# Kernel tuning notes

Hardware: AMD Instinct MI355X
Metric: run time of the kernel (lower is better)

The kernel has to match this reference:

```python
import jax, jax.numpy as jnp
import numpy as np

DIM = 64  # per-head key dim; temp = sqrt(DIM)
B, S = 32, 2048  # flattened batch*heads, seq_len


def setup_inputs() -> dict:
    key = jax.random.key(0)
    kq, kk, kv = jax.random.split(key, 3)
    q = jax.random.normal(kq, (B, S, DIM), dtype=jnp.float32)
    k = jax.random.normal(kk, (B, S, DIM), dtype=jnp.float32)
    v = jax.random.normal(kv, (B, S, DIM), dtype=jnp.float32)
    return {"q": q, "k": k, "v": v}


def reference(q, k, v):
    temp = np.sqrt(DIM).astype(np.float32)
    # attn = bmm(q, k^T) / sqrt(dim): [B, Sq, Sk]
    attn = jnp.einsum("bqd,bkd->bqk", q, k) / temp
    # softmax over key dim (the view/softmax(dim=1)/view trick == softmax over last axis)
    attn = jax.nn.softmax(attn, axis=-1)
    # dropout p=0.0 -> identity
    out = jnp.einsum("bqk,bkd->bqd", attn, v)
    return out
```

## Files before the change

kernel.cpp:

```cpp
#include <hip/hip_runtime.h>
#include <hip/hip_bf16.h>

#define S_ 2048
#define D_ 64
#define BM 128
#define BN 128
#define KSTR 72
#define VSTR 136

typedef __attribute__((ext_vector_type(8))) short bf16x8;
typedef __attribute__((ext_vector_type(16))) float f32x16;

__device__ __forceinline__ unsigned int cvtpk(float lo, float hi) {
    unsigned int r;
    asm("v_cvt_pk_bf16_f32 %0, %1, %2" : "=v"(r) : "v"(lo), "v"(hi));
    return r;
}

__global__ __launch_bounds__(256, 2) void fattn(const float* __restrict__ q,
                                                const float* __restrict__ kg,
                                                const float* __restrict__ vg,
                                                float* __restrict__ out) {
    __shared__ ushort Kt[BN * KSTR];
    __shared__ ushort Vs[BN * KSTR];
    __shared__ ushort Vt[D_ * VSTR];

    const int tid  = threadIdx.x;
    const int wid  = tid >> 6;
    const int lane = tid & 63;
    const int lq   = lane & 31;
    const int lh   = lane >> 5;

    const int bid   = blockIdx.x;
    const int xcd   = bid & 7;
    const int slot  = bid >> 3;
    const int batch = xcd + 8 * (slot >> 4);
    const int qtile = slot & 15;

    const float* qp = q  + (size_t)batch * S_ * D_;
    const float* kp = kg + (size_t)batch * S_ * D_;
    const float* vp = vg + (size_t)batch * S_ * D_;

    const float SC = 0.18033688011112042f;
    const int qrow = qtile * BM + wid * 32 + lq;
    bf16x8 qf[4];
    {
        const float* qr = qp + (size_t)qrow * D_ + 8 * lh;
#pragma unroll
        for (int kk = 0; kk < 4; ++kk) {
            union { bf16x8 v; unsigned int u[4]; } uq;
#pragma unroll
            for (int j = 0; j < 4; ++j)
                uq.u[j] = cvtpk(qr[kk * 16 + 2 * j] * SC, qr[kk * 16 + 2 * j + 1] * SC);
            qf[kk] = uq.v;
        }
    }

    f32x16 O[2];
#pragma unroll
    for (int md = 0; md < 2; ++md)
#pragma unroll
        for (int j = 0; j < 16; ++j) O[md][j] = 0.f;
    float l = 0.f;

#pragma unroll
    for (int p = 0; p < 4; ++p) {
        const int c = p * 256 + tid;
        const float4 a = *(const float4*)(kp + c * 8);
        const float4 b = *(const float4*)(kp + c * 8 + 4);
        uint4 ok;
        ok.x = cvtpk(a.x, a.y); ok.y = cvtpk(a.z, a.w);
        ok.z = cvtpk(b.x, b.y); ok.w = cvtpk(b.z, b.w);
        *(uint4*)(&Kt[(c >> 3) * KSTR + (c & 7) * 8]) = ok;
        const float4 x = *(const float4*)(vp + c * 8);
        const float4 y = *(const float4*)(vp + c * 8 + 4);
        uint4 ov;
        ov.x = cvtpk(x.x, x.y); ov.y = cvtpk(x.z, x.w);
        ov.z = cvtpk(y.x, y.y); ov.w = cvtpk(y.z, y.w);
        *(uint4*)(&Vs[(c >> 3) * KSTR + (c & 7) * 8]) = ov;
    }

    float4 ka[4], kb[4], va[4], vb[4];

    for (int kt = 0; kt < S_; kt += BN) {
        __syncthreads();
        const bool more = (kt + BN < S_);

        if (more) {
            const float* ks = kp + (size_t)(kt + BN) * D_;
            const float* vs = vp + (size_t)(kt + BN) * D_;
#pragma unroll
            for (int p = 0; p < 4; ++p) {
                const int c8 = (p * 256 + tid) * 8;
                ka[p] = *(const float4*)(ks + c8);
                kb[p] = *(const float4*)(ks + c8 + 4);
                va[p] = *(const float4*)(vs + c8);
                vb[p] = *(const float4*)(vs + c8 + 4);
            }
        }

        f32x16 sa[4];
#pragma unroll
        for (int mt = 0; mt < 4; ++mt) {
            const ushort* krow = &Kt[(mt * 32 + lq) * KSTR + 8 * lh];
            f32x16 acc;
#pragma unroll
            for (int j = 0; j < 16; ++j) acc[j] = 0.f;
#pragma unroll
            for (int kk = 0; kk < 4; ++kk) {
                const bf16x8 kf = *(const bf16x8*)(krow + kk * 16);
                acc = __builtin_amdgcn_mfma_f32_32x32x16_bf16(kf, qf[kk], acc, 0, 0, 0);
            }
            sa[mt] = acc;
        }

        {
            const int d = tid & 63;
#pragma unroll
            for (int j = 0; j < 4; ++j) {
                const int chunk = (tid >> 6) + 4 * j;
                const ushort* src = &Vs[(chunk * 8) * KSTR + d];
                const unsigned int x0 = src[0 * KSTR], x1 = src[1 * KSTR];
                const unsigned int x2 = src[2 * KSTR], x3 = src[3 * KSTR];
                const unsigned int x4 = src[4 * KSTR], x5 = src[5 * KSTR];
                const unsigned int x6 = src[6 * KSTR], x7 = src[7 * KSTR];
                uint4 o;
                o.x = x0 | (x1 << 16); o.y = x2 | (x3 << 16);
                o.z = x4 | (x5 << 16); o.w = x6 | (x7 << 16);
                *(uint4*)(&Vt[d * VSTR + chunk * 8]) = o;
            }
        }

        float r0 = 0.f, r1 = 0.f, r2 = 0.f, r3 = 0.f;
#pragma unroll
        for (int g = 0; g < 4; ++g)
#pragma unroll
            for (int j = 0; j < 16; j += 4) {
                const float e0 = __builtin_amdgcn_exp2f(sa[g][j]);
                const float e1 = __builtin_amdgcn_exp2f(sa[g][j + 1]);
                const float e2 = __builtin_amdgcn_exp2f(sa[g][j + 2]);
                const float e3 = __builtin_amdgcn_exp2f(sa[g][j + 3]);
                sa[g][j] = e0; sa[g][j + 1] = e1; sa[g][j + 2] = e2; sa[g][j + 3] = e3;
                r0 += e0; r1 += e1; r2 += e2; r3 += e3;
            }
        float rs = (r0 + r1) + (r2 + r3);
        rs += __shfl_xor(rs, 32, 64);
        l += rs;

        __syncthreads();

#pragma unroll
        for (int g = 0; g < 4; ++g) {
#pragma unroll
            for (int h = 0; h < 2; ++h) {
                union { bf16x8 v; unsigned int u[4]; } pf;
#pragma unroll
                for (int i = 0; i < 4; ++i)
                    pf.u[i] = cvtpk(sa[g][h * 8 + 2 * i], sa[g][h * 8 + 2 * i + 1]);
                const int koff = g * 32 + h * 16 + 4 * lh;
#pragma unroll
                for (int md = 0; md < 2; ++md) {
                    const ushort* vb2 = &Vt[(md * 32 + lq) * VSTR + koff];
                    union { bf16x8 v; uint2 p[2]; } vf;
                    vf.p[0] = *(const uint2*)(vb2);
                    vf.p[1] = *(const uint2*)(vb2 + 8);
                    O[md] = __builtin_amdgcn_mfma_f32_32x32x16_bf16(vf.v, pf.v, O[md], 0, 0, 0);
                }
            }
        }

        if (more) {
#pragma unroll
            for (int p = 0; p < 4; ++p) {
                const int c = p * 256 + tid;
                uint4 ok;
                ok.x = cvtpk(ka[p].x, ka[p].y); ok.y = cvtpk(ka[p].z, ka[p].w);
                ok.z = cvtpk(kb[p].x, kb[p].y); ok.w = cvtpk(kb[p].z, kb[p].w);
                *(uint4*)(&Kt[(c >> 3) * KSTR + (c & 7) * 8]) = ok;
                uint4 ov;
                ov.x = cvtpk(va[p].x, va[p].y); ov.y = cvtpk(va[p].z, va[p].w);
                ov.z = cvtpk(vb[p].x, vb[p].y); ov.w = cvtpk(vb[p].z, vb[p].w);
                *(uint4*)(&Vs[(c >> 3) * KSTR + (c & 7) * 8]) = ov;
            }
        }
    }

    const float linv = 1.0f / l;
    float* op = out + (size_t)batch * S_ * D_ + (size_t)qrow * D_;
#pragma unroll
    for (int md = 0; md < 2; ++md) {
#pragma unroll
        for (int r4 = 0; r4 < 4; ++r4) {
            const int d = md * 32 + r4 * 8 + 4 * lh;
            float4 st;
            st.x = O[md][r4 * 4 + 0] * linv;
            st.y = O[md][r4 * 4 + 1] * linv;
            st.z = O[md][r4 * 4 + 2] * linv;
            st.w = O[md][r4 * 4 + 3] * linv;
            *(float4*)(op + d) = st;
        }
    }
}

extern "C" void kernel_launch(void* const* d_in, const int* in_sizes, int n_in,
                              void* d_out, int out_size, void* d_ws, size_t ws_size,
                              hipStream_t stream) {
    const float* q = (const float*)d_in[0];
    const float* k = (const float*)d_in[1];
    const float* v = (const float*)d_in[2];
    float* o = (float*)d_out;

    fattn<<<dim3(512), dim3(256), 0, stream>>>(q, k, v, o);
}
```

Before: 130.4 us.

## Transpose V during global loads and double-buffer the transposed V tile

Result: slower. 133.5 us (+2.4%).

```diff
diff --git a/kernel.cpp b/kernel.cpp
--- a/kernel.cpp
+++ b/kernel.cpp
@@ -22,14 +22,15 @@
                                                 const float* __restrict__ vg,
                                                 float* __restrict__ out) {
     __shared__ ushort Kt[BN * KSTR];
-    __shared__ ushort Vs[BN * KSTR];
-    __shared__ ushort Vt[D_ * VSTR];
+    __shared__ ushort Vt[2][D_ * VSTR];
 
     const int tid  = threadIdx.x;
     const int wid  = tid >> 6;
     const int lane = tid & 63;
     const int lq   = lane & 31;
     const int lh   = lane >> 5;
+    const int d63  = tid & 63;
+    const int k4   = tid >> 6;
 
     const int bid   = blockIdx.x;
     const int xcd   = bid & 7;
@@ -72,19 +73,26 @@
         ok.x = cvtpk(a.x, a.y); ok.y = cvtpk(a.z, a.w);
         ok.z = cvtpk(b.x, b.y); ok.w = cvtpk(b.z, b.w);
         *(uint4*)(&Kt[(c >> 3) * KSTR + (c & 7) * 8]) = ok;
-        const float4 x = *(const float4*)(vp + c * 8);
-        const float4 y = *(const float4*)(vp + c * 8 + 4);
-        uint4 ov;
-        ov.x = cvtpk(x.x, x.y); ov.y = cvtpk(x.z, x.w);
-        ov.z = cvtpk(y.x, y.y); ov.w = cvtpk(y.z, y.w);
-        *(uint4*)(&Vs[(c >> 3) * KSTR + (c & 7) * 8]) = ov;
-    }
-
-    float4 ka[4], kb[4], va[4], vb[4];
+    }
+#pragma unroll
+    for (int j = 0; j < 4; ++j) {
+        const int ko = k4 + 4 * j;
+        float x[8];
+#pragma unroll
+        for (int i = 0; i < 8; ++i) x[i] = vp[(ko * 8 + i) * D_ + d63];
+        uint4 o;
+        o.x = cvtpk(x[0], x[1]); o.y = cvtpk(x[2], x[3]);
+        o.z = cvtpk(x[4], x[5]); o.w = cvtpk(x[6], x[7]);
+        *(uint4*)(&Vt[0][d63 * VSTR + ko * 8]) = o;
+    }
+
+    float4 ka[4], kb[4];
+    float  vv[4][8];
 
     for (int kt = 0; kt < S_; kt += BN) {
         __syncthreads();
         const bool more = (kt + BN < S_);
+        const int  b    = (kt >> 7) & 1;
 
         if (more) {
             const float* ks = kp + (size_t)(kt + BN) * D_;
@@ -94,9 +102,12 @@
                 const int c8 = (p * 256 + tid) * 8;
                 ka[p] = *(const float4*)(ks + c8);
                 kb[p] = *(const float4*)(ks + c8 + 4);
-                va[p] = *(const float4*)(vs + c8);
-                vb[p] = *(const float4*)(vs + c8 + 4);
-            }
+            }
+#pragma unroll
+            for (int j = 0; j < 4; ++j)
+#pragma unroll
+                for (int i = 0; i < 8; ++i)
+                    vv[j][i] = vs[((k4 + 4 * j) * 8 + i) * D_ + d63];
         }
 
         f32x16 sa[4];
@@ -112,23 +123,6 @@
                 acc = __builtin_amdgcn_mfma_f32_32x32x16_bf16(kf, qf[kk], acc, 0, 0, 0);
             }
             sa[mt] = acc;
-        }
-
-        {
-            const int d = tid & 63;
-#pragma unroll
-            for (int j = 0; j < 4; ++j) {
-                const int chunk = (tid >> 6) + 4 * j;
-                const ushort* src = &Vs[(chunk * 8) * KSTR + d];
-                const unsigned int x0 = src[0 * KSTR], x1 = src[1 * KSTR];
-                const unsigned int x2 = src[2 * KSTR], x3 = src[3 * KSTR];
-                const unsigned int x4 = src[4 * KSTR], x5 = src[5 * KSTR];
-                const unsigned int x6 = src[6 * KSTR], x7 = src[7 * KSTR];
-                uint4 o;
-                o.x = x0 | (x1 << 16); o.y = x2 | (x3 << 16);
-                o.z = x4 | (x5 << 16); o.w = x6 | (x7 << 16);
-                *(uint4*)(&Vt[d * VSTR + chunk * 8]) = o;
-            }
         }
 
         float r0 = 0.f, r1 = 0.f, r2 = 0.f, r3 = 0.f;
@@ -160,7 +154,7 @@
                 const int koff = g * 32 + h * 16 + 4 * lh;
 #pragma unroll
                 for (int md = 0; md < 2; ++md) {
-                    const ushort* vb2 = &Vt[(md * 32 + lq) * VSTR + koff];
+                    const ushort* vb2 = &Vt[b][(md * 32 + lq) * VSTR + koff];
                     union { bf16x8 v; uint2 p[2]; } vf;
                     vf.p[0] = *(const uint2*)(vb2);
                     vf.p[1] = *(const uint2*)(vb2 + 8);
@@ -177,10 +171,15 @@
                 ok.x = cvtpk(ka[p].x, ka[p].y); ok.y = cvtpk(ka[p].z, ka[p].w);
                 ok.z = cvtpk(kb[p].x, kb[p].y); ok.w = cvtpk(kb[p].z, kb[p].w);
                 *(uint4*)(&Kt[(c >> 3) * KSTR + (c & 7) * 8]) = ok;
-                uint4 ov;
-                ov.x = cvtpk(va[p].x, va[p].y); ov.y = cvtpk(va[p].z, va[p].w);
-                ov.z = cvtpk(vb[p].x, vb[p].y); ov.w = cvtpk(vb[p].z, vb[p].w);
-                *(uint4*)(&Vs[(c >> 3) * KSTR + (c & 7) * 8]) = ov;
+            }
+            ushort* vtn = &Vt[b ^ 1][0];
+#pragma unroll
+            for (int j = 0; j < 4; ++j) {
+                const int ko = k4 + 4 * j;
+                uint4 o;
+                o.x = cvtpk(vv[j][0], vv[j][1]); o.y = cvtpk(vv[j][2], vv[j][3]);
+                o.z = cvtpk(vv[j][4], vv[j][5]); o.w = cvtpk(vv[j][6], vv[j][7]);
+                *(uint4*)(&vtn[d63 * VSTR + ko * 8]) = o;
             }
         }
     }
```
